# Optimization experiments

Hardware: AMD Instinct MI355X
Metric: run time of the kernel (lower is better)

## Reference

```python
import jax, jax.numpy as jnp
import numpy as np

N = 4096
D = 256
H = 8
E = 131072
NEG = -1e30  # stands in for -inf; keeps grads NaN-free


def setup_inputs() -> dict:
    key = jax.random.key(0)
    ks = jax.random.split(key, 8)
    s = 1.0 / np.sqrt(D)
    return {
        "x": jax.random.normal(ks[0], (N, D), dtype=jnp.float32),
        "edge_index": jax.random.randint(ks[1], (2, E), 0, N, dtype=jnp.int32),
        "Wq": jax.random.normal(ks[2], (D, D), dtype=jnp.float32) * s,
        "Wk": jax.random.normal(ks[3], (D, D), dtype=jnp.float32) * s,
        "Wv": jax.random.normal(ks[4], (D, D), dtype=jnp.float32) * s,
        "Wo": jax.random.normal(ks[5], (D, D), dtype=jnp.float32) * s,
        "bo": jnp.zeros((D,), dtype=jnp.float32),
        "gamma": jnp.ones((D,), dtype=jnp.float32),
        "beta": jnp.zeros((D,), dtype=jnp.float32),
    }


def reference(x, edge_index, Wq, Wk, Wv, Wo, bo, gamma, beta):
    n, d_model = x.shape
    d_h = d_model // H
    scale = jnp.sqrt(jnp.float32(d_h))

    # mask: True = blocked. Diagonal and graph edges (dst attends to src) unblocked.
    mask = jnp.ones((n, n), dtype=bool)
    diag = jnp.arange(n)
    mask = mask.at[diag, diag].set(False)
    src, dst = edge_index[0], edge_index[1]
    mask = mask.at[dst, src].set(False)

    # projections: torch Linear computes x @ W.T
    Q = (x @ Wq.T).reshape(n, H, d_h).transpose(1, 0, 2)  # [H, N, d_h]
    K = (x @ Wk.T).reshape(n, H, d_h).transpose(1, 0, 2)
    V = (x @ Wv.T).reshape(n, H, d_h).transpose(1, 0, 2)

    scores = jnp.einsum("hnd,hmd->hnm", Q, K) / scale      # [H, N, N]
    scores = jnp.where(mask[None, :, :], NEG, scores)
    attn = jax.nn.softmax(scores, axis=-1)
    attn = jnp.nan_to_num(attn, nan=0.0)

    out = jnp.einsum("hnm,hmd->hnd", attn, V)              # [H, N, d_h]
    out = out.transpose(1, 0, 2).reshape(n, d_model)
    out = out @ Wo.T + bo

    # LayerNorm(x + out), eps=1e-5
    h = x + out
    mu = jnp.mean(h, axis=-1, keepdims=True)
    var = jnp.var(h, axis=-1, keepdims=True)
    return (h - mu) * jax.lax.rsqrt(var + 1e-5) * gamma + beta
```

## Files before the change

### kernel.cpp

```cpp
#include <hip/hip_runtime.h>

#define D_MODEL 256
#define N_HEADS 8
#define D_HEAD 32
#define MAXN 192

typedef __attribute__((ext_vector_type(8))) short bf16x8;
typedef __attribute__((ext_vector_type(4))) float f32x4;

__device__ __forceinline__ unsigned short f2bf(float f) {
    union { float f; unsigned int u; } v; v.f = f;
    unsigned int r = v.u + 0x7fff + ((v.u >> 16) & 1);
    return (unsigned short)(r >> 16);
}
__device__ __forceinline__ float bf2f(unsigned short u) {
    union { unsigned int u; float f; } v; v.u = ((unsigned int)u) << 16;
    return v.f;
}

__global__ void convert_kernel(const float* __restrict__ x,
                               const float* __restrict__ W0, const float* __restrict__ W1,
                               const float* __restrict__ W2, const float* __restrict__ W3,
                               unsigned short* __restrict__ xb,
                               unsigned short* __restrict__ O0, unsigned short* __restrict__ O1,
                               unsigned short* __restrict__ O2, unsigned short* __restrict__ O3) {
    const int XV = (4096 * 256) / 4;
    int i = blockIdx.x * blockDim.x + threadIdx.x;
    const float* src;
    unsigned short* dst;
    int k;
    if (i < XV) {
        src = x; dst = xb; k = i;
    } else {
        int i2 = i - XV;
        int z = i2 >> 14;
        k = i2 & 16383;
        src = (z == 0) ? W0 : (z == 1) ? W1 : (z == 2) ? W2 : W3;
        dst = (z == 0) ? O0 : (z == 1) ? O1 : (z == 2) ? O2 : O3;
    }
    float4 v = *(const float4*)(src + (size_t)k * 4);
    ushort4 o;
    o.x = f2bf(v.x); o.y = f2bf(v.y); o.z = f2bf(v.z); o.w = f2bf(v.w);
    *(ushort4*)(dst + (size_t)k * 4) = o;
}

__global__ void set_edges_kernel(const int* __restrict__ ei,
                                 unsigned long long* __restrict__ mask,
                                 int E, int n) {
    int e = blockIdx.x * blockDim.x + threadIdx.x;
    int wpr = n >> 6;
    if (e < n)
        atomicOr(&mask[(size_t)e * wpr + (e >> 6)], 1ULL << (e & 63));
    if (e < E) {
        int src = ei[e];
        int dst = ei[E + e];
        atomicOr(&mask[(size_t)dst * wpr + (src >> 6)], 1ULL << (src & 63));
    }
}

template <int BF16OUT>
__device__ __forceinline__ void gemm_bf16_body(const unsigned short* __restrict__ A,
                                               const unsigned short* __restrict__ B,
                                               float* __restrict__ C,
                                               unsigned short* __restrict__ Cb,
                                               int bx, int by) {
    __shared__ short Alds[128][72];
    __shared__ short Blds[64][72];
    int t = threadIdx.x;
    int wave = t >> 6, lane = t & 63;
    int wr = wave >> 1, wc = wave & 1;
    int lr = t >> 3;
    int lk = (t & 7) << 3;

    const unsigned short* Abase = A + ((size_t)(by * 128 + lr)) * D_MODEL + lk;
    const unsigned short* Bbase = B + ((size_t)(bx * 64 + lr)) * D_MODEL + lk;

    int fm = lane & 15;
    int fk = (lane >> 4) << 3;

    f32x4 acc[4][2];
#pragma unroll
    for (int r = 0; r < 4; ++r)
#pragma unroll
        for (int c = 0; c < 2; ++c) acc[r][c] = (f32x4){0.f, 0.f, 0.f, 0.f};

    for (int k0 = 0; k0 < D_MODEL; k0 += 64) {
        *(uint4*)&Alds[lr][lk]      = *(const uint4*)(Abase + k0);
        *(uint4*)&Alds[lr + 32][lk] = *(const uint4*)(Abase + 32 * D_MODEL + k0);
        *(uint4*)&Alds[lr + 64][lk] = *(const uint4*)(Abase + 64 * D_MODEL + k0);
        *(uint4*)&Alds[lr + 96][lk] = *(const uint4*)(Abase + 96 * D_MODEL + k0);
        *(uint4*)&Blds[lr][lk]      = *(const uint4*)(Bbase + k0);
        *(uint4*)&Blds[lr + 32][lk] = *(const uint4*)(Bbase + 32 * D_MODEL + k0);
        __syncthreads();
#pragma unroll
        for (int ks = 0; ks < 64; ks += 32) {
            bf16x8 af[4], bf[2];
#pragma unroll
            for (int r = 0; r < 4; ++r)
                af[r] = *(const bf16x8*)&Alds[wr * 64 + r * 16 + fm][ks + fk];
#pragma unroll
            for (int c = 0; c < 2; ++c)
                bf[c] = *(const bf16x8*)&Blds[wc * 32 + c * 16 + fm][ks + fk];
#pragma unroll
            for (int r = 0; r < 4; ++r)
#pragma unroll
                for (int c = 0; c < 2; ++c)
                    acc[r][c] = __builtin_amdgcn_mfma_f32_16x16x32_bf16(
                        af[r], bf[c], acc[r][c], 0, 0, 0);
        }
        __syncthreads();
    }

    int orow0 = by * 128 + wr * 64 + ((lane >> 4) << 2);
    int ocol0 = bx * 64 + wc * 32 + (lane & 15);
#pragma unroll
    for (int r = 0; r < 4; ++r)
#pragma unroll
        for (int c = 0; c < 2; ++c)
#pragma unroll
            for (int q = 0; q < 4; ++q) {
                size_t idx = (size_t)(orow0 + r * 16 + q) * D_MODEL + ocol0 + c * 16;
                if (BF16OUT) Cb[idx] = f2bf(acc[r][c][q]);
                else         C[idx]  = acc[r][c][q];
            }
}

__global__ __launch_bounds__(256) void gemm_qkv_kernel(
        const unsigned short* __restrict__ xb,
        const unsigned short* __restrict__ Wq, const unsigned short* __restrict__ Wk,
        const unsigned short* __restrict__ Wv,
        unsigned short* __restrict__ Qb, unsigned short* __restrict__ Kb,
        unsigned short* __restrict__ Vb) {
    const unsigned short* B = (blockIdx.z == 0) ? Wq : (blockIdx.z == 1) ? Wk : Wv;
    unsigned short* Cb = (blockIdx.z == 0) ? Qb : (blockIdx.z == 1) ? Kb : Vb;
    gemm_bf16_body<1>(xb, B, nullptr, Cb, blockIdx.x, blockIdx.y);
}

__global__ __launch_bounds__(256) void gemm_o_kernel(
        const unsigned short* __restrict__ Ob, const unsigned short* __restrict__ Wo,
        float* __restrict__ C) {
    gemm_bf16_body<0>(Ob, Wo, C, nullptr, blockIdx.x, blockIdx.y);
}

__global__ __launch_bounds__(64) void attn_kernel(
        const unsigned short* __restrict__ Qb, const unsigned short* __restrict__ Kb,
        const unsigned short* __restrict__ Vb,
        const unsigned long long* __restrict__ mask,
        unsigned short* __restrict__ Ob, int n) {
    int dst = blockIdx.x;
    int L = threadIdx.x;
    int wpr = n >> 6;

    __shared__ int nbr[MAXN + 16];
    __shared__ float s_lds[N_HEADS][MAXN];

    unsigned long long w = (L < wpr) ? mask[(size_t)dst * wpr + L] : 0ULL;
    int c = __popcll(w);
    int xs = c;
#pragma unroll
    for (int o = 1; o < 64; o <<= 1) {
        int y = __shfl_up(xs, o, 64);
        if (L >= o) xs += y;
    }
    int pos = xs - c;
    while (w) {
        int b = __builtin_ctzll(w);
        w &= w - 1;
        if (pos < MAXN) nbr[pos] = (L << 6) + b;
        ++pos;
    }
    int cnt = __shfl(xs, 63, 64);
    if (cnt > MAXN) cnt = MAXN;
    int nb = (cnt + 15) & ~15;
    __syncthreads();
    int last = nbr[cnt - 1];
    if (L < nb - cnt) nbr[cnt + L] = last;
    __syncthreads();

    int col = L & 15;
    int kq = L >> 4;
    bf16x8 qf = (bf16x8){0, 0, 0, 0, 0, 0, 0, 0};
    if (col < N_HEADS)
        qf = *(const bf16x8*)(Qb + (size_t)dst * D_MODEL + col * D_HEAD + kq * 8);
    const bf16x8 zf = (bf16x8){0, 0, 0, 0, 0, 0, 0, 0};
    const float inv_scale = 0.17677669529663687f;

    for (int b0 = 0; b0 < nb; b0 += 16) {
        int nj = nbr[b0 + col];
        const unsigned short* krow = Kb + (size_t)nj * D_MODEL + kq * 8;
        f32x4 c0 = (f32x4){0.f, 0.f, 0.f, 0.f};
        f32x4 c1 = (f32x4){0.f, 0.f, 0.f, 0.f};
#pragma unroll
        for (int kb = 0; kb < 8; kb += 2) {
            bf16x8 a0 = *(const bf16x8*)(krow + kb * 32);
            bf16x8 a1 = *(const bf16x8*)(krow + kb * 32 + 32);
            bf16x8 bop0 = (col == kb)     ? qf : zf;
            bf16x8 bop1 = (col == kb + 1) ? qf : zf;
            c0 = __builtin_amdgcn_mfma_f32_16x16x32_bf16(a0, bop0, c0, 0, 0, 0);
            c1 = __builtin_amdgcn_mfma_f32_16x16x32_bf16(a1, bop1, c1, 0, 0, 0);
        }
        if (col < N_HEADS) {
            int jr = b0 + kq * 4;
            float4 o;
            float s0 = (c0[0] + c1[0]) * inv_scale;
            float s1 = (c0[1] + c1[1]) * inv_scale;
            float s2 = (c0[2] + c1[2]) * inv_scale;
            float s3 = (c0[3] + c1[3]) * inv_scale;
            o.x = (jr + 0 < cnt) ? s0 : -1e30f;
            o.y = (jr + 1 < cnt) ? s1 : -1e30f;
            o.z = (jr + 2 < cnt) ? s2 : -1e30f;
            o.w = (jr + 3 < cnt) ? s3 : -1e30f;
            *(float4*)&s_lds[col][jr] = o;
        }
    }
    __syncthreads();

    int h = L >> 3, i = L & 7;
    float m = -1e30f;
    for (int j0 = i * 4; j0 < nb; j0 += 32) {
        float4 v = *(const float4*)&s_lds[h][j0];
        m = fmaxf(m, fmaxf(fmaxf(v.x, v.y), fmaxf(v.z, v.w)));
    }
    m = fmaxf(m, __shfl_xor(m, 1, 8));
    m = fmaxf(m, __shfl_xor(m, 2, 8));
    m = fmaxf(m, __shfl_xor(m, 4, 8));
    float l = 0.f;
    for (int j0 = i * 4; j0 < nb; j0 += 32) {
        float4 v = *(const float4*)&s_lds[h][j0];
        float4 e;
        e.x = __expf(v.x - m); e.y = __expf(v.y - m);
        e.z = __expf(v.z - m); e.w = __expf(v.w - m);
        *(float4*)&s_lds[h][j0] = e;
        l += (e.x + e.y) + (e.z + e.w);
    }
    l += __shfl_xor(l, 1, 8);
    l += __shfl_xor(l, 2, 8);
    l += __shfl_xor(l, 4, 8);
    __syncthreads();

    f32x4 acc = (f32x4){0.f, 0.f, 0.f, 0.f};
    const unsigned short* vb = Vb + 4 * L;
    for (int j = 0; j < nb; j += 4) {
        float4 wv = *(const float4*)&s_lds[h][j];
        int j0 = nbr[j], j1 = nbr[j + 1], j2 = nbr[j + 2], j3 = nbr[j + 3];
        uint2 r0 = *(const uint2*)(vb + (size_t)j0 * D_MODEL);
        uint2 r1 = *(const uint2*)(vb + (size_t)j1 * D_MODEL);
        uint2 r2 = *(const uint2*)(vb + (size_t)j2 * D_MODEL);
        uint2 r3 = *(const uint2*)(vb + (size_t)j3 * D_MODEL);
        acc[0] += wv.x * bf2f((unsigned short)(r0.x & 0xffff));
        acc[1] += wv.x * bf2f((unsigned short)(r0.x >> 16));
        acc[2] += wv.x * bf2f((unsigned short)(r0.y & 0xffff));
        acc[3] += wv.x * bf2f((unsigned short)(r0.y >> 16));
        acc[0] += wv.y * bf2f((unsigned short)(r1.x & 0xffff));
        acc[1] += wv.y * bf2f((unsigned short)(r1.x >> 16));
        acc[2] += wv.y * bf2f((unsigned short)(r1.y & 0xffff));
        acc[3] += wv.y * bf2f((unsigned short)(r1.y >> 16));
        acc[0] += wv.z * bf2f((unsigned short)(r2.x & 0xffff));
        acc[1] += wv.z * bf2f((unsigned short)(r2.x >> 16));
        acc[2] += wv.z * bf2f((unsigned short)(r2.y & 0xffff));
        acc[3] += wv.z * bf2f((unsigned short)(r2.y >> 16));
        acc[0] += wv.w * bf2f((unsigned short)(r3.x & 0xffff));
        acc[1] += wv.w * bf2f((unsigned short)(r3.x >> 16));
        acc[2] += wv.w * bf2f((unsigned short)(r3.y & 0xffff));
        acc[3] += wv.w * bf2f((unsigned short)(r3.y >> 16));
    }
    float rl = 1.f / l;
    ushort4 o;
    o.x = f2bf(acc[0] * rl); o.y = f2bf(acc[1] * rl);
    o.z = f2bf(acc[2] * rl); o.w = f2bf(acc[3] * rl);
    *(ushort4*)(Ob + (size_t)dst * D_MODEL + 4 * L) = o;
}

__global__ __launch_bounds__(256) void ln_kernel(
        const float* __restrict__ x, const float* __restrict__ proj,
        const float* __restrict__ bo, const float* __restrict__ gamma,
        const float* __restrict__ beta, float* __restrict__ out) {
    int row = blockIdx.x;
    int t = threadIdx.x;
    float h = x[(size_t)row * D_MODEL + t] + proj[(size_t)row * D_MODEL + t] + bo[t];

    __shared__ float red[4];
    __shared__ float red2[4];
    int wave = t >> 6, lane = t & 63;

    float s = h;
#pragma unroll
    for (int o = 32; o; o >>= 1) s += __shfl_down(s, o, 64);
    if (lane == 0) red[wave] = s;
    __syncthreads();
    float mu = (red[0] + red[1] + red[2] + red[3]) * (1.f / 256.f);

    float d = h - mu;
    float s2 = d * d;
#pragma unroll
    for (int o = 32; o; o >>= 1) s2 += __shfl_down(s2, o, 64);
    if (lane == 0) red2[wave] = s2;
    __syncthreads();
    float var = (red2[0] + red2[1] + red2[2] + red2[3]) * (1.f / 256.f);

    out[(size_t)row * D_MODEL + t] = d * rsqrtf(var + 1e-5f) * gamma[t] + beta[t];
}

extern "C" void kernel_launch(void* const* d_in, const int* in_sizes, int n_in,
                              void* d_out, int out_size, void* d_ws, size_t ws_size,
                              hipStream_t stream) {
    const float* x     = (const float*)d_in[0];
    const int*   ei    = (const int*)  d_in[1];
    const float* Wq    = (const float*)d_in[2];
    const float* Wk    = (const float*)d_in[3];
    const float* Wv    = (const float*)d_in[4];
    const float* Wo    = (const float*)d_in[5];
    const float* bo    = (const float*)d_in[6];
    const float* gamma = (const float*)d_in[7];
    const float* beta  = (const float*)d_in[8];
    float* out = (float*)d_out;

    int n = in_sizes[0] / D_MODEL;
    int E = in_sizes[1] / 2;

    char* ws = (char*)d_ws;
    size_t off = 0;
    unsigned long long* mask = (unsigned long long*)(ws + off);
    size_t mask_bytes = (size_t)n * (n >> 6) * sizeof(unsigned long long);
    off += mask_bytes;
    unsigned short* xb  = (unsigned short*)(ws + off); off += (size_t)n * D_MODEL * 2;
    unsigned short* Wqb = (unsigned short*)(ws + off); off += D_MODEL * D_MODEL * 2;
    unsigned short* Wkb = (unsigned short*)(ws + off); off += D_MODEL * D_MODEL * 2;
    unsigned short* Wvb = (unsigned short*)(ws + off); off += D_MODEL * D_MODEL * 2;
    unsigned short* Wob = (unsigned short*)(ws + off); off += D_MODEL * D_MODEL * 2;
    unsigned short* Qb  = (unsigned short*)(ws + off); off += (size_t)n * D_MODEL * 2;
    unsigned short* Kb  = (unsigned short*)(ws + off); off += (size_t)n * D_MODEL * 2;
    unsigned short* Vb  = (unsigned short*)(ws + off); off += (size_t)n * D_MODEL * 2;
    unsigned short* Ob  = (unsigned short*)(ws + off); off += (size_t)n * D_MODEL * 2;
    float* proj = (float*)(ws + off); off += (size_t)n * D_MODEL * sizeof(float);

    hipMemsetAsync(mask, 0, mask_bytes, stream);

    int conv_blocks = ((4096 * 256) / 4 + 4 * 16384) / 256;
    convert_kernel<<<conv_blocks, 256, 0, stream>>>(x, Wq, Wk, Wv, Wo,
                                                    xb, Wqb, Wkb, Wvb, Wob);

    set_edges_kernel<<<(E + 255) / 256, 256, 0, stream>>>(ei, mask, E, n);

    dim3 gq(D_MODEL / 64, n / 128, 3);
    gemm_qkv_kernel<<<gq, 256, 0, stream>>>(xb, Wqb, Wkb, Wvb, Qb, Kb, Vb);

    attn_kernel<<<n, 64, 0, stream>>>(Qb, Kb, Vb, mask, Ob, n);

    dim3 go(D_MODEL / 64, n / 128);
    gemm_o_kernel<<<go, 256, 0, stream>>>(Ob, Wob, proj);

    ln_kernel<<<n, 256, 0, stream>>>(x, proj, bo, gamma, beta, out);
}
```

Before: 118.8 us.

## Fuse fp32-to-bf16 conversion into GEMMs and merge output projection with LayerNorm

Removes the separate conversion kernel by converting fp32 x and weights to bf16 while staging tiles into LDS inside the QKV GEMM and the output GEMM. The output projection is restructured so each block computes full 64-row by 256-column tiles. LayerNorm is then applied in-block from an LDS staging buffer, which eliminates the fp32 proj round-trip and two launches. In exchange, the fused O-GEMM grid is only 64 blocks and every block re-reads and re-converts all of Wo. The variance now uses a single-pass E[x^2]-mu^2 form.

```diff
diff --git a/kernel.cpp b/kernel.cpp
--- a/kernel.cpp
+++ b/kernel.cpp
@@ -17,31 +17,14 @@
     union { unsigned int u; float f; } v; v.u = ((unsigned int)u) << 16;
     return v.f;
 }
-
-__global__ void convert_kernel(const float* __restrict__ x,
-                               const float* __restrict__ W0, const float* __restrict__ W1,
-                               const float* __restrict__ W2, const float* __restrict__ W3,
-                               unsigned short* __restrict__ xb,
-                               unsigned short* __restrict__ O0, unsigned short* __restrict__ O1,
-                               unsigned short* __restrict__ O2, unsigned short* __restrict__ O3) {
-    const int XV = (4096 * 256) / 4;
-    int i = blockIdx.x * blockDim.x + threadIdx.x;
-    const float* src;
-    unsigned short* dst;
-    int k;
-    if (i < XV) {
-        src = x; dst = xb; k = i;
-    } else {
-        int i2 = i - XV;
-        int z = i2 >> 14;
-        k = i2 & 16383;
-        src = (z == 0) ? W0 : (z == 1) ? W1 : (z == 2) ? W2 : W3;
-        dst = (z == 0) ? O0 : (z == 1) ? O1 : (z == 2) ? O2 : O3;
-    }
-    float4 v = *(const float4*)(src + (size_t)k * 4);
-    ushort4 o;
-    o.x = f2bf(v.x); o.y = f2bf(v.y); o.z = f2bf(v.z); o.w = f2bf(v.w);
-    *(ushort4*)(dst + (size_t)k * 4) = o;
+__device__ __forceinline__ void pack8(const float* __restrict__ p, short* __restrict__ dst) {
+    float4 u0 = *(const float4*)p;
+    float4 u1 = *(const float4*)(p + 4);
+    ushort4 a, b;
+    a.x = f2bf(u0.x); a.y = f2bf(u0.y); a.z = f2bf(u0.z); a.w = f2bf(u0.w);
+    b.x = f2bf(u1.x); b.y = f2bf(u1.y); b.z = f2bf(u1.z); b.w = f2bf(u1.w);
+    *(ushort4*)dst = a;
+    *(ushort4*)(dst + 4) = b;
 }
 
 __global__ void set_edges_kernel(const int* __restrict__ ei,
@@ -58,12 +41,16 @@
     }
 }
 
-template <int BF16OUT>
-__device__ __forceinline__ void gemm_bf16_body(const unsigned short* __restrict__ A,
-                                               const unsigned short* __restrict__ B,
-                                               float* __restrict__ C,
-                                               unsigned short* __restrict__ Cb,
-                                               int bx, int by) {
+__global__ __launch_bounds__(256) void gemm_qkv_kernel(
+        const float* __restrict__ x,
+        const float* __restrict__ Wq, const float* __restrict__ Wk,
+        const float* __restrict__ Wv,
+        unsigned short* __restrict__ Qb, unsigned short* __restrict__ Kb,
+        unsigned short* __restrict__ Vb) {
+    const float* B = (blockIdx.z == 0) ? Wq : (blockIdx.z == 1) ? Wk : Wv;
+    unsigned short* Cb = (blockIdx.z == 0) ? Qb : (blockIdx.z == 1) ? Kb : Vb;
+    int bx = blockIdx.x, by = blockIdx.y;
+
     __shared__ short Alds[128][72];
     __shared__ short Blds[64][72];
     int t = threadIdx.x;
@@ -72,8 +59,8 @@
     int lr = t >> 3;
     int lk = (t & 7) << 3;
 
-    const unsigned short* Abase = A + ((size_t)(by * 128 + lr)) * D_MODEL + lk;
-    const unsigned short* Bbase = B + ((size_t)(bx * 64 + lr)) * D_MODEL + lk;
+    const float* Abase = x + ((size_t)(by * 128 + lr)) * D_MODEL + lk;
+    const float* Bbase = B + ((size_t)(bx * 64 + lr)) * D_MODEL + lk;
 
     int fm = lane & 15;
     int fk = (lane >> 4) << 3;
@@ -85,12 +72,12 @@
         for (int c = 0; c < 2; ++c) acc[r][c] = (f32x4){0.f, 0.f, 0.f, 0.f};
 
     for (int k0 = 0; k0 < D_MODEL; k0 += 64) {
-        *(uint4*)&Alds[lr][lk]      = *(const uint4*)(Abase + k0);
-        *(uint4*)&Alds[lr + 32][lk] = *(const uint4*)(Abase + 32 * D_MODEL + k0);
-        *(uint4*)&Alds[lr + 64][lk] = *(const uint4*)(Abase + 64 * D_MODEL + k0);
-        *(uint4*)&Alds[lr + 96][lk] = *(const uint4*)(Abase + 96 * D_MODEL + k0);
-        *(uint4*)&Blds[lr][lk]      = *(const uint4*)(Bbase + k0);
-        *(uint4*)&Blds[lr + 32][lk] = *(const uint4*)(Bbase + 32 * D_MODEL + k0);
+        pack8(Abase + k0,               &Alds[lr][lk]);
+        pack8(Abase + 32 * D_MODEL + k0, &Alds[lr + 32][lk]);
+        pack8(Abase + 64 * D_MODEL + k0, &Alds[lr + 64][lk]);
+        pack8(Abase + 96 * D_MODEL + k0, &Alds[lr + 96][lk]);
+        pack8(Bbase + k0,               &Blds[lr][lk]);
+        pack8(Bbase + 32 * D_MODEL + k0, &Blds[lr + 32][lk]);
         __syncthreads();
 #pragma unroll
         for (int ks = 0; ks < 64; ks += 32) {
@@ -118,28 +105,9 @@
 #pragma unroll
         for (int c = 0; c < 2; ++c)
 #pragma unroll
-            for (int q = 0; q < 4; ++q) {
-                size_t idx = (size_t)(orow0 + r * 16 + q) * D_MODEL + ocol0 + c * 16;
-                if (BF16OUT) Cb[idx] = f2bf(acc[r][c][q]);
-                else         C[idx]  = acc[r][c][q];
-            }
-}
-
-__global__ __launch_bounds__(256) void gemm_qkv_kernel(
-        const unsigned short* __restrict__ xb,
-        const unsigned short* __restrict__ Wq, const unsigned short* __restrict__ Wk,
-        const unsigned short* __restrict__ Wv,
-        unsigned short* __restrict__ Qb, unsigned short* __restrict__ Kb,
-        unsigned short* __restrict__ Vb) {
-    const unsigned short* B = (blockIdx.z == 0) ? Wq : (blockIdx.z == 1) ? Wk : Wv;
-    unsigned short* Cb = (blockIdx.z == 0) ? Qb : (blockIdx.z == 1) ? Kb : Vb;
-    gemm_bf16_body<1>(xb, B, nullptr, Cb, blockIdx.x, blockIdx.y);
-}
-
-__global__ __launch_bounds__(256) void gemm_o_kernel(
-        const unsigned short* __restrict__ Ob, const unsigned short* __restrict__ Wo,
-        float* __restrict__ C) {
-    gemm_bf16_body<0>(Ob, Wo, C, nullptr, blockIdx.x, blockIdx.y);
+            for (int q = 0; q < 4; ++q)
+                Cb[(size_t)(orow0 + r * 16 + q) * D_MODEL + ocol0 + c * 16] =
+                    f2bf(acc[r][c][q]);
 }
 
 __global__ __launch_bounds__(64) void attn_kernel(
@@ -271,34 +239,90 @@
     *(ushort4*)(Ob + (size_t)dst * D_MODEL + 4 * L) = o;
 }
 
-__global__ __launch_bounds__(256) void ln_kernel(
-        const float* __restrict__ x, const float* __restrict__ proj,
-        const float* __restrict__ bo, const float* __restrict__ gamma,
-        const float* __restrict__ beta, float* __restrict__ out) {
-    int row = blockIdx.x;
+struct SMemO {
+    union {
+        struct { short A[64][72]; short B[256][72]; } st;
+        float c[64][260];
+    };
+};
+
+__global__ __launch_bounds__(256) void gemm_o_ln_kernel(
+        const unsigned short* __restrict__ Ob, const float* __restrict__ Wo,
+        const float* __restrict__ x, const float* __restrict__ bo,
+        const float* __restrict__ gamma, const float* __restrict__ beta,
+        float* __restrict__ out) {
+    __shared__ SMemO sm;
+    int by = blockIdx.x;
     int t = threadIdx.x;
-    float h = x[(size_t)row * D_MODEL + t] + proj[(size_t)row * D_MODEL + t] + bo[t];
-
-    __shared__ float red[4];
-    __shared__ float red2[4];
     int wave = t >> 6, lane = t & 63;
-
-    float s = h;
-#pragma unroll
-    for (int o = 32; o; o >>= 1) s += __shfl_down(s, o, 64);
-    if (lane == 0) red[wave] = s;
-    __syncthreads();
-    float mu = (red[0] + red[1] + red[2] + red[3]) * (1.f / 256.f);
-
-    float d = h - mu;
-    float s2 = d * d;
-#pragma unroll
-    for (int o = 32; o; o >>= 1) s2 += __shfl_down(s2, o, 64);
-    if (lane == 0) red2[wave] = s2;
-    __syncthreads();
-    float var = (red2[0] + red2[1] + red2[2] + red2[3]) * (1.f / 256.f);
-
-    out[(size_t)row * D_MODEL + t] = d * rsqrtf(var + 1e-5f) * gamma[t] + beta[t];
+    int lr = t >> 3;
+    int lk = (t & 7) << 3;
+
+    const unsigned short* Abase = Ob + ((size_t)(by * 64 + lr)) * D_MODEL + lk;
+    int fm = lane & 15;
+    int fk = (lane >> 4) << 3;
+
+    f32x4 acc[16];
+#pragma unroll
+    for (int ct = 0; ct < 16; ++ct) acc[ct] = (f32x4){0.f, 0.f, 0.f, 0.f};
+
+    for (int k0 = 0; k0 < D_MODEL; k0 += 64) {
+        *(uint4*)&sm.st.A[lr][lk]      = *(const uint4*)(Abase + k0);
+        *(uint4*)&sm.st.A[lr + 32][lk] = *(const uint4*)(Abase + 32 * D_MODEL + k0);
+#pragma unroll
+        for (int j = 0; j < 8; ++j)
+            pack8(Wo + ((size_t)(lr + 32 * j)) * D_MODEL + k0 + lk,
+                  &sm.st.B[lr + 32 * j][lk]);
+        __syncthreads();
+#pragma unroll
+        for (int ks = 0; ks < 64; ks += 32) {
+            bf16x8 af = *(const bf16x8*)&sm.st.A[wave * 16 + fm][ks + fk];
+#pragma unroll
+            for (int ct = 0; ct < 16; ++ct) {
+                bf16x8 bf = *(const bf16x8*)&sm.st.B[ct * 16 + fm][ks + fk];
+                acc[ct] = __builtin_amdgcn_mfma_f32_16x16x32_bf16(af, bf, acc[ct], 0, 0, 0);
+            }
+        }
+        __syncthreads();
+    }
+
+    int rr0 = wave * 16 + ((lane >> 4) << 2);
+#pragma unroll
+    for (int ct = 0; ct < 16; ++ct)
+#pragma unroll
+        for (int q = 0; q < 4; ++q)
+            sm.c[rr0 + q][ct * 16 + (lane & 15)] = acc[ct][q];
+    __syncthreads();
+
+    float4 bo4 = *(const float4*)(bo + lane * 4);
+    float4 g4  = *(const float4*)(gamma + lane * 4);
+    float4 be4 = *(const float4*)(beta + lane * 4);
+    for (int rr = 0; rr < 16; ++rr) {
+        int r = wave * 16 + rr;
+        int grow = by * 64 + r;
+        float4 p = *(const float4*)&sm.c[r][lane * 4];
+        float4 xv = *(const float4*)(x + (size_t)grow * D_MODEL + lane * 4);
+        float hx = p.x + xv.x + bo4.x;
+        float hy = p.y + xv.y + bo4.y;
+        float hz = p.z + xv.z + bo4.z;
+        float hw = p.w + xv.w + bo4.w;
+        float s  = (hx + hy) + (hz + hw);
+        float s2 = (hx * hx + hy * hy) + (hz * hz + hw * hw);
+#pragma unroll
+        for (int o = 32; o; o >>= 1) {
+            s  += __shfl_xor(s, o, 64);
+            s2 += __shfl_xor(s2, o, 64);
+        }
+        float mu = s * (1.f / 256.f);
+        float var = s2 * (1.f / 256.f) - mu * mu;
+        float rstd = rsqrtf(var + 1e-5f);
+        float4 o4;
+        o4.x = (hx - mu) * rstd * g4.x + be4.x;
+        o4.y = (hy - mu) * rstd * g4.y + be4.y;
+        o4.z = (hz - mu) * rstd * g4.z + be4.z;
+        o4.w = (hw - mu) * rstd * g4.w + be4.w;
+        *(float4*)(out + (size_t)grow * D_MODEL + lane * 4) = o4;
+    }
 }
 
 extern "C" void kernel_launch(void* const* d_in, const int* in_sizes, int n_in,
@@ -323,32 +347,18 @@
     unsigned long long* mask = (unsigned long long*)(ws + off);
     size_t mask_bytes = (size_t)n * (n >> 6) * sizeof(unsigned long long);
     off += mask_bytes;
-    unsigned short* xb  = (unsigned short*)(ws + off); off += (size_t)n * D_MODEL * 2;
-    unsigned short* Wqb = (unsigned short*)(ws + off); off += D_MODEL * D_MODEL * 2;
-    unsigned short* Wkb = (unsigned short*)(ws + off); off += D_MODEL * D_MODEL * 2;
-    unsigned short* Wvb = (unsigned short*)(ws + off); off += D_MODEL * D_MODEL * 2;
-    unsigned short* Wob = (unsigned short*)(ws + off); off += D_MODEL * D_MODEL * 2;
-    unsigned short* Qb  = (unsigned short*)(ws + off); off += (size_t)n * D_MODEL * 2;
-    unsigned short* Kb  = (unsigned short*)(ws + off); off += (size_t)n * D_MODEL * 2;
-    unsigned short* Vb  = (unsigned short*)(ws + off); off += (size_t)n * D_MODEL * 2;
-    unsigned short* Ob  = (unsigned short*)(ws + off); off += (size_t)n * D_MODEL * 2;
-    float* proj = (float*)(ws + off); off += (size_t)n * D_MODEL * sizeof(float);
+    unsigned short* Qb = (unsigned short*)(ws + off); off += (size_t)n * D_MODEL * 2;
+    unsigned short* Kb = (unsigned short*)(ws + off); off += (size_t)n * D_MODEL * 2;
+    unsigned short* Vb = (unsigned short*)(ws + off); off += (size_t)n * D_MODEL * 2;
+    unsigned short* Ob = (unsigned short*)(ws + off); off += (size_t)n * D_MODEL * 2;
 
     hipMemsetAsync(mask, 0, mask_bytes, stream);
-
-    int conv_blocks = ((4096 * 256) / 4 + 4 * 16384) / 256;
-    convert_kernel<<<conv_blocks, 256, 0, stream>>>(x, Wq, Wk, Wv, Wo,
-                                                    xb, Wqb, Wkb, Wvb, Wob);
-
     set_edges_kernel<<<(E + 255) / 256, 256, 0, stream>>>(ei, mask, E, n);
 
     dim3 gq(D_MODEL / 64, n / 128, 3);
-    gemm_qkv_kernel<<<gq, 256, 0, stream>>>(xb, Wqb, Wkb, Wvb, Qb, Kb, Vb);
+    gemm_qkv_kernel<<<gq, 256, 0, stream>>>(x, Wq, Wk, Wv, Qb, Kb, Vb);
 
     attn_kernel<<<n, 64, 0, stream>>>(Qb, Kb, Vb, mask, Ob, n);
 
-    dim3 go(D_MODEL / 64, n / 128);
-    gemm_o_kernel<<<go, 256, 0, stream>>>(Ob, Wob, proj);
-
-    ln_kernel<<<n, 256, 0, stream>>>(x, proj, bo, gamma, beta, out);
-}
+    gemm_o_ln_kernel<<<n / 64, 256, 0, stream>>>(Ob, Wo, x, bo, gamma, beta, out);
+}
```

Measured after the change: 134.9 us. 13.5% more time.
